# Kernel tuning notes

Measured on AMD Instinct MI355X. Metric: run time of the kernel, lower is better.

Reference implementation:

```python
import jax, jax.numpy as jnp
import numpy as np

B, L, E, H = 2, 2048, 1024, 16
HD = E // H  # 64
THETA = 10000.0


def setup_inputs() -> dict:
    key = jax.random.key(0)
    ks = jax.random.split(key, 9)
    s = 1.0 / np.sqrt(E)
    return {
        "x": jax.random.normal(ks[0], (B, L, E), jnp.float32),
        "Wq": jax.random.normal(ks[1], (E, E), jnp.float32) * s,
        "bq": jax.random.normal(ks[2], (E,), jnp.float32) * 0.01,
        "Wk": jax.random.normal(ks[3], (E, E), jnp.float32) * s,
        "bk": jax.random.normal(ks[4], (E,), jnp.float32) * 0.01,
        "Wv": jax.random.normal(ks[5], (E, E), jnp.float32) * s,
        "bv": jax.random.normal(ks[6], (E,), jnp.float32) * 0.01,
        "Wo": jax.random.normal(ks[7], (E, E), jnp.float32) * s,
        "bo": jax.random.normal(ks[8], (E,), jnp.float32) * 0.01,
    }


def _rope_tables(seq_len, dim, dtype):
    # lucidrains RotaryEmbedding: inv_freq over even indices, each freq repeated twice (interleaved)
    inv_freq = 1.0 / (THETA ** (jnp.arange(0, dim, 2, dtype=jnp.float32) / dim))
    freqs = jnp.arange(seq_len, dtype=jnp.float32)[:, None] * inv_freq[None, :]  # [L, dim/2]
    freqs = jnp.repeat(freqs, 2, axis=-1)  # [L, dim] -> f0,f0,f1,f1,...
    return jnp.cos(freqs).astype(dtype), jnp.sin(freqs).astype(dtype)


def _rotate_half(x):
    # interleaved pairs (x0, x1) -> (-x1, x0)
    x2 = x.reshape(*x.shape[:-1], -1, 2)
    x2 = jnp.stack([-x2[..., 1], x2[..., 0]], axis=-1)
    return x2.reshape(x.shape)


def _apply_rope(x, cos, sin):
    # x: [B, H, L, HD]; cos/sin: [L, HD]
    return x * cos[None, None] + _rotate_half(x) * sin[None, None]


def reference(x, Wq, bq, Wk, bk, Wv, bv, Wo, bo):
    b, l, e = x.shape
    q = (x @ Wq.T + bq).reshape(b, l, H, HD).transpose(0, 2, 1, 3)
    k = (x @ Wk.T + bk).reshape(b, l, H, HD).transpose(0, 2, 1, 3)
    v = (x @ Wv.T + bv).reshape(b, l, H, HD).transpose(0, 2, 1, 3)

    cos, sin = _rope_tables(l, HD, x.dtype)
    q = _apply_rope(q, cos, sin)
    k = _apply_rope(k, cos, sin)

    scale = 1.0 / np.sqrt(HD)
    scores = jnp.einsum("bhsd,bhed->bhse", q, k) * scale  # [B,H,L,L]
    attn = jax.nn.softmax(scores, axis=-1)
    out = jnp.einsum("bhse,bhed->bhsd", attn, v)  # [B,H,L,HD]
    out = out.transpose(0, 2, 1, 3).reshape(b, l, e)
    return out @ Wo.T + bo
```

## Files before the change

kernel.cpp:

```cpp
#include <hip/hip_runtime.h>

typedef unsigned short u16;
typedef __bf16 bf16x8 __attribute__((ext_vector_type(8)));
typedef float f32x4 __attribute__((ext_vector_type(4)));

#define LOG2E 1.4426950408889634f
#define EXP2(x) __builtin_amdgcn_exp2f(x)
#define NFM (-11.0f * LOG2E)

__device__ __forceinline__ u16 f2bf(float f) {
  unsigned int u = __float_as_uint(f);
  u += 0x7fffu + ((u >> 16) & 1u);
  return (u16)(u >> 16);
}

__device__ __forceinline__ void gld16(u16* lds, const u16* g) {
  __builtin_amdgcn_global_load_lds((const __attribute__((address_space(1))) unsigned int*)g,
                                   (__attribute__((address_space(3))) unsigned int*)lds,
                                   16, 0, 0);
}

__device__ __forceinline__ bf16x8 ldsv(const u16* p) {
  return *(const bf16x8*)p;
}

union U8 { uint4 u; bf16x8 v; };

__global__ __launch_bounds__(256) void k_prep(const float* __restrict__ x,
    const float* __restrict__ wq, const float* __restrict__ wk,
    const float* __restrict__ wv, const float* __restrict__ wo,
    u16* __restrict__ xb, u16* __restrict__ wqkvb, u16* __restrict__ wob,
    float* __restrict__ cosT, float* __restrict__ sinT) {
  unsigned gid = blockIdx.x * 256u + threadIdx.x;
  if (gid >= 2097152u) {
    unsigned t = gid - 2097152u;
    int l = t >> 5, i = t & 31;
    float inv = powf(10000.0f, -(float)i * (1.0f / 32.0f));
    float ang = (float)l * inv;
    float s, c;
    sincosf(ang, &s, &c);
    cosT[t] = c;
    sinT[t] = s;
    return;
  }
  const float4* src;
  u16* dst;
  unsigned off;
  if (gid < 1048576u)      { src = (const float4*)x;  dst = xb;              off = gid; }
  else if (gid < 1310720u) { src = (const float4*)wq; dst = wqkvb;           off = gid - 1048576u; }
  else if (gid < 1572864u) { src = (const float4*)wk; dst = wqkvb + 1048576; off = gid - 1310720u; }
  else if (gid < 1835008u) { src = (const float4*)wv; dst = wqkvb + 2097152; off = gid - 1572864u; }
  else                     { src = (const float4*)wo; dst = wob;             off = gid - 1835008u; }
  float4 f = src[off];
  ushort4 o;
  o.x = f2bf(f.x); o.y = f2bf(f.y); o.z = f2bf(f.z); o.w = f2bf(f.w);
  ((ushort4*)dst)[off] = o;
}

__device__ __forceinline__ void stage_tile(const u16* __restrict__ A, const u16* __restrict__ B,
                                           int m0, int n0, int kb, u16* dst) {
  const int tid = threadIdx.x;
#pragma unroll
  for (int it = 0; it < 4; ++it) {
    int idx = it * 256 + tid;
    int row = idx >> 3, c8 = idx & 7;
    int sc = c8 ^ (row & 7);
    gld16(dst + idx * 8,        A + (long)(m0 + row) * 1024 + kb + sc * 8);
    gld16(dst + 8192 + idx * 8, B + (long)(n0 + row) * 1024 + kb + sc * 8);
  }
}

__device__ __forceinline__ void gemm_loop(const u16* __restrict__ A, const u16* __restrict__ B,
                                          int m0, int n0, u16* S, f32x4 acc[4][4]) {
  const int tid = threadIdx.x;
  const int lane = tid & 63, wave = tid >> 6;
  const int quad = lane >> 4, l16 = lane & 15;
  const int wm = wave & 1, wn = wave >> 1;
  const int sw = l16 & 7;

#pragma unroll
  for (int i = 0; i < 4; ++i)
#pragma unroll
    for (int j = 0; j < 4; ++j)
      acc[i][j] = (f32x4){0.f, 0.f, 0.f, 0.f};

  stage_tile(A, B, m0, n0, 0, S);
  __syncthreads();

  for (int kt = 0; kt < 16; ++kt) {
    const int off = (kt & 1) << 14;
    const u16* As = S + off;
    const u16* Bs = S + off + 8192;
    if (kt < 15)
      stage_tile(A, B, m0, n0, (kt + 1) * 64, S + (off ^ 16384));
#pragma unroll
    for (int kk = 0; kk < 2; ++kk) {
      int ch = (kk * 4 + quad) ^ sw;
      bf16x8 a[4], b[4];
#pragma unroll
      for (int i = 0; i < 4; ++i)
        a[i] = ldsv(As + (wm * 64 + i * 16 + l16) * 64 + ch * 8);
#pragma unroll
      for (int j = 0; j < 4; ++j)
        b[j] = ldsv(Bs + (wn * 64 + j * 16 + l16) * 64 + ch * 8);
#pragma unroll
      for (int i = 0; i < 4; ++i)
#pragma unroll
        for (int j = 0; j < 4; ++j)
          acc[i][j] = __builtin_amdgcn_mfma_f32_16x16x32_bf16(a[i], b[j], acc[i][j], 0, 0, 0);
    }
    __syncthreads();
  }
}

__global__ __launch_bounds__(256) void k_qkv(const u16* __restrict__ xb, const u16* __restrict__ wqkvb,
    const float* __restrict__ bq, const float* __restrict__ bk, const float* __restrict__ bv,
    const float* __restrict__ cosT, const float* __restrict__ sinT,
    u16* __restrict__ Qg, u16* __restrict__ Kg, u16* __restrict__ VTg) {
  __shared__ __align__(16) u16 S[32768];
  f32x4 acc[4][4];
  int m0 = blockIdx.y * 128, n0 = blockIdx.x * 128;
  gemm_loop(xb, wqkvb, m0, n0, S, acc);

  const int tid = threadIdx.x, lane = tid & 63, wave = tid >> 6;
  const int quad = lane >> 4, l16 = lane & 15;
  const int wm = wave & 1, wn = wave >> 1;
  const int qsel = n0 >> 10;
  const int b = m0 >> 11;
  const int mb0 = m0 & 2047;

  if (qsel < 2) {
    const float* bp = qsel ? bk : bq;
#pragma unroll
    for (int j = 0; j < 4; ++j) {
      int nl = wn * 64 + j * 16 + l16;
      int n = n0 + nl;
      int fcol = n & 1023;
      int d = fcol & 63;
      int pi = d >> 1;
      float bias = bp[fcol];
      float sgn = (d & 1) ? 1.0f : -1.0f;
#pragma unroll
      for (int i = 0; i < 4; ++i) {
#pragma unroll
        for (int r = 0; r < 4; ++r) {
          int ml = wm * 64 + i * 16 + quad * 4 + r;
          int l = mb0 + ml;
          float v = acc[i][j][r] + bias;
          float partner = __shfl_xor(v, 1);
          float c = cosT[l * 32 + pi], s = sinT[l * 32 + pi];
          float o = fmaf(v, c, sgn * partner * s);
          if (qsel == 0) o *= 0.125f;
          S[ml * 132 + nl] = f2bf(o);
        }
      }
    }
    __syncthreads();
    u16* dstb = (qsel == 0) ? Qg : Kg;
#pragma unroll
    for (int t = 0; t < 16; ++t) {
      int idx = t * 256 + tid;
      int ml = idx >> 5, c4 = idx & 31;
      int n = n0 + c4 * 4;
      int h = (n & 1023) >> 6;
      int d = n & 63;
      *(uint2*)(dstb + (((long)b * 16 + h) * 2048 + mb0 + ml) * 64 + d) =
          *(const uint2*)(S + ml * 132 + c4 * 4);
    }
  } else {
#pragma unroll
    for (int j = 0; j < 4; ++j) {
      int nl = wn * 64 + j * 16 + l16;
      float bias = bv[(n0 + nl) & 1023];
#pragma unroll
      for (int i = 0; i < 4; ++i) {
        int mb = wm * 64 + i * 16 + quad * 4;
        unsigned u0 = (unsigned)f2bf(acc[i][j][0] + bias) | ((unsigned)f2bf(acc[i][j][1] + bias) << 16);
        unsigned u1 = (unsigned)f2bf(acc[i][j][2] + bias) | ((unsigned)f2bf(acc[i][j][3] + bias) << 16);
        *(uint2*)(S + nl * 132 + mb) = make_uint2(u0, u1);
      }
    }
    __syncthreads();
#pragma unroll
    for (int t = 0; t < 16; ++t) {
      int idx = t * 256 + tid;
      int nl = idx >> 5, c4 = idx & 31;
      int vcol = (n0 & 1023) + nl;
      int h = vcol >> 6, d = vcol & 63;
      *(uint2*)(VTg + (((long)b * 16 + h) * 64 + d) * 2048 + mb0 + c4 * 4) =
          *(const uint2*)(S + nl * 132 + c4 * 4);
    }
  }
}

__global__ __launch_bounds__(256, 2) void k_attn(const u16* __restrict__ Qg, const u16* __restrict__ Kg,
    const u16* __restrict__ VTg, u16* __restrict__ Ctx) {
  __shared__ __align__(16) char smem[65536];
  u16* Ks = (u16*)smem;
  u16* Vs0 = (u16*)(smem + 32768);
  const int tid = threadIdx.x, lane = tid & 63, wave = tid >> 6;
  const int quad = lane >> 4, l16 = lane & 15;
  const int wm = wave & 1, wsn = wave >> 1;
  const int sw = l16 & 7;
  const int bh = blockIdx.y;
  const int m0 = blockIdx.x * 128;
  const u16* Qb = Qg + (long)bh * 2048 * 64;
  const u16* Kb = Kg + (long)bh * 2048 * 64;
  const u16* Vb = VTg + (long)bh * 64 * 2048;

  bf16x8 qf[4][2];
#pragma unroll
  for (int mt = 0; mt < 4; ++mt)
#pragma unroll
    for (int kk = 0; kk < 2; ++kk)
      qf[mt][kk] = *(const bf16x8*)(Qb + (long)(m0 + wm * 64 + mt * 16 + l16) * 64 + kk * 32 + quad * 8);

  U8 ones;
  {
    unsigned w = (l16 == 0) ? 0x3F803F80u : 0u;
    ones.u = make_uint4(w, w, w, w);
  }
  const f32x4 zero4 = {0.f, 0.f, 0.f, 0.f};

  f32x4 oacc[4][4];
  f32x4 racc[4];
#pragma unroll
  for (int dt = 0; dt < 4; ++dt)
#pragma unroll
    for (int mt = 0; mt < 4; ++mt)
      oacc[dt][mt] = (f32x4){0.f, 0.f, 0.f, 0.f};
#pragma unroll
  for (int mt = 0; mt < 4; ++mt) racc[mt] = (f32x4){0.f, 0.f, 0.f, 0.f};

  const int r7 = l16 & 7;
  const int qh = quad >> 1;
  const int qo = (quad & 1) * 4;

#pragma unroll
  for (int it = 0; it < 4; ++it) {
    int idx = it * 256 + tid;
    int row = idx >> 4, c16 = idx & 15;
    int sc = (c16 & 8) | ((c16 & 7) ^ (row & 7));
    gld16(Vs0 + idx * 8, Vb + (long)row * 2048 + sc * 8);
  }
#pragma unroll
  for (int it = 0; it < 4; ++it) {
    int idx = it * 256 + tid;
    int row = idx >> 3, c8 = idx & 7;
    int sc = c8 ^ (row & 7);
    gld16(Ks + idx * 8, Kb + (long)row * 64 + sc * 8);
  }
  __syncthreads();

  for (int st = 0; st < 16; ++st) {
    const int cur = st & 1;
    const u16* Ksc = Ks + cur * 8192;
    u16* Ksa = Ks + (cur ^ 1) * 8192;
    const u16* Vsc = Vs0 + cur * 8192;
    u16* Vsa = Vs0 + (cur ^ 1) * 8192;

    if (st < 15) {
      int s0n = (st + 1) * 128;
#pragma unroll
      for (int it = 0; it < 4; ++it) {
        int idx = it * 256 + tid;
        int row = idx >> 4, c16 = idx & 15;
        int sc = (c16 & 8) | ((c16 & 7) ^ (row & 7));
        gld16(Vsa + idx * 8, Vb + (long)row * 2048 + s0n + sc * 8);
      }
#pragma unroll
      for (int it = 0; it < 4; ++it) {
        int idx = it * 256 + tid;
        int row = idx >> 3, c8 = idx & 7;
        int sc = c8 ^ (row & 7);
        gld16(Ksa + idx * 8, Kb + (long)(s0n + row) * 64 + sc * 8);
      }
    }

    f32x4 sacc[4][4];
    {
      int ch = quad ^ sw;
      bf16x8 kf[4];
#pragma unroll
      for (int ct = 0; ct < 4; ++ct)
        kf[ct] = ldsv(Ksc + (wsn * 64 + ct * 16 + l16) * 64 + ch * 8);
#pragma unroll
      for (int ct = 0; ct < 4; ++ct)
#pragma unroll
        for (int mt = 0; mt < 4; ++mt)
          sacc[ct][mt] = __builtin_amdgcn_mfma_f32_16x16x32_bf16(kf[ct], qf[mt][0], zero4, 0, 0, 0);
    }
    {
      int ch = (4 + quad) ^ sw;
      bf16x8 kf[4];
#pragma unroll
      for (int ct = 0; ct < 4; ++ct)
        kf[ct] = ldsv(Ksc + (wsn * 64 + ct * 16 + l16) * 64 + ch * 8);
#pragma unroll
      for (int ct = 0; ct < 4; ++ct)
#pragma unroll
        for (int mt = 0; mt < 4; ++mt)
          sacc[ct][mt] = __builtin_amdgcn_mfma_f32_16x16x32_bf16(kf[ct], qf[mt][1], sacc[ct][mt], 0, 0, 0);
    }

#pragma unroll
    for (int c = 0; c < 2; ++c) {
      unsigned pk[2][4][2];
#pragma unroll
      for (int t = 0; t < 2; ++t) {
        int ct = c * 2 + t;
#pragma unroll
        for (int mt = 0; mt < 4; ++mt) {
          unsigned b[4];
#pragma unroll
          for (int r = 0; r < 4; ++r) {
            float e = EXP2(fmaf(sacc[ct][mt][r], LOG2E, NFM));
            b[r] = __float_as_uint(e);
          }
          pk[t][mt][0] = __builtin_amdgcn_perm(b[1], b[0], 0x07060302u);
          pk[t][mt][1] = __builtin_amdgcn_perm(b[3], b[2], 0x07060302u);
        }
      }
      const int slo = (4 * c + qh) ^ r7;
      const int shi = (4 * c + qh + 2) ^ r7;
#pragma unroll
      for (int dt = 0; dt < 4; ++dt) {
        const u16* vrow = Vsc + (dt * 16 + l16) * 128 + wsn * 64;
        uint2 lo = *(const uint2*)(vrow + slo * 8 + qo);
        uint2 hi = *(const uint2*)(vrow + shi * 8 + qo);
        U8 vfu; vfu.u = make_uint4(lo.x, lo.y, hi.x, hi.y);
#pragma unroll
        for (int mt = 0; mt < 4; ++mt) {
          U8 pfu; pfu.u = make_uint4(pk[0][mt][0], pk[0][mt][1], pk[1][mt][0], pk[1][mt][1]);
          oacc[dt][mt] = __builtin_amdgcn_mfma_f32_16x16x32_bf16(vfu.v, pfu.v, oacc[dt][mt], 0, 0, 0);
        }
      }
#pragma unroll
      for (int mt = 0; mt < 4; ++mt) {
        U8 pfu; pfu.u = make_uint4(pk[0][mt][0], pk[0][mt][1], pk[1][mt][0], pk[1][mt][1]);
        racc[mt] = __builtin_amdgcn_mfma_f32_16x16x32_bf16(ones.v, pfu.v, racc[mt], 0, 0, 0);
      }
    }

    __syncthreads();
  }

  float rs[4];
#pragma unroll
  for (int mt = 0; mt < 4; ++mt) rs[mt] = racc[mt][0];

  float* mbuf = (float*)smem;
  if (wsn == 1) {
#pragma unroll
    for (int dt = 0; dt < 4; ++dt)
#pragma unroll
      for (int mt = 0; mt < 4; ++mt)
#pragma unroll
        for (int r = 0; r < 4; ++r)
          mbuf[(wm * 68 + dt * 16 + mt * 4 + r) * 64 + lane] = oacc[dt][mt][r];
#pragma unroll
    for (int mt = 0; mt < 4; ++mt)
      mbuf[(wm * 68 + 64 + mt) * 64 + lane] = rs[mt];
  }
  __syncthreads();
  if (wsn == 0) {
#pragma unroll
    for (int dt = 0; dt < 4; ++dt)
#pragma unroll
      for (int mt = 0; mt < 4; ++mt)
#pragma unroll
        for (int r = 0; r < 4; ++r)
          oacc[dt][mt][r] += mbuf[(wm * 68 + dt * 16 + mt * 4 + r) * 64 + lane];
#pragma unroll
    for (int mt = 0; mt < 4; ++mt) {
      rs[mt] += mbuf[(wm * 68 + 64 + mt) * 64 + lane];
      rs[mt] += __shfl_xor(rs[mt], 16);
      rs[mt] += __shfl_xor(rs[mt], 32);
    }
    const int b = bh >> 4, h = bh & 15;
#pragma unroll
    for (int mt = 0; mt < 4; ++mt) {
      float inv = 1.0f / rs[mt];
      int tok = m0 + wm * 64 + mt * 16 + l16;
      u16* cp = Ctx + ((long)(b * 2048 + tok)) * 1024 + h * 64 + quad * 4;
#pragma unroll
      for (int dt = 0; dt < 4; ++dt) {
        float o0 = oacc[dt][mt][0] * inv, o1 = oacc[dt][mt][1] * inv;
        float o2 = oacc[dt][mt][2] * inv, o3 = oacc[dt][mt][3] * inv;
        unsigned u0 = (unsigned)f2bf(o0) | ((unsigned)f2bf(o1) << 16);
        unsigned u1 = (unsigned)f2bf(o2) | ((unsigned)f2bf(o3) << 16);
        *(uint2*)(cp + dt * 16) = make_uint2(u0, u1);
      }
    }
  }
}

__device__ __forceinline__ void stage_tile64(const u16* __restrict__ A, const u16* __restrict__ B,
                                             int m0, int n0, int kb, u16* dst) {
  const int tid = threadIdx.x;
#pragma unroll
  for (int it = 0; it < 2; ++it) {
    int idx = it * 256 + tid;
    int row = idx >> 3, c8 = idx & 7;
    int sc = c8 ^ (row & 7);
    gld16(dst + idx * 8, A + (long)(m0 + row) * 1024 + kb + sc * 8);
  }
#pragma unroll
  for (int it = 0; it < 4; ++it) {
    int idx = it * 256 + tid;
    int row = idx >> 3, c8 = idx & 7;
    int sc = c8 ^ (row & 7);
    gld16(dst + 4096 + idx * 8, B + (long)(n0 + row) * 1024 + kb + sc * 8);
  }
}

__global__ __launch_bounds__(256) void k_out(const u16* __restrict__ Ctx, const u16* __restrict__ wob,
    const float* __restrict__ bo, float* __restrict__ out) {
  __shared__ __align__(16) u16 S[24576];
  const int tid = threadIdx.x, lane = tid & 63, wave = tid >> 6;
  const int quad = lane >> 4, l16 = lane & 15;
  const int wm = wave & 1, wn = wave >> 1;
  const int sw = l16 & 7;
  int m0 = blockIdx.y * 64, n0 = blockIdx.x * 128;

  f32x4 acc[2][4];
#pragma unroll
  for (int i = 0; i < 2; ++i)
#pragma unroll
    for (int j = 0; j < 4; ++j)
      acc[i][j] = (f32x4){0.f, 0.f, 0.f, 0.f};

  stage_tile64(Ctx, wob, m0, n0, 0, S);
  __syncthreads();

  for (int kt = 0; kt < 16; ++kt) {
    const int off = (kt & 1) * 12288;
    const u16* As = S + off;
    const u16* Bs = S + off + 4096;
    if (kt < 15)
      stage_tile64(Ctx, wob, m0, n0, (kt + 1) * 64, S + (off ^ 12288));
#pragma unroll
    for (int kk = 0; kk < 2; ++kk) {
      int ch = (kk * 4 + quad) ^ sw;
      bf16x8 a[2], b[4];
#pragma unroll
      for (int i = 0; i < 2; ++i)
        a[i] = ldsv(As + (wm * 32 + i * 16 + l16) * 64 + ch * 8);
#pragma unroll
      for (int j = 0; j < 4; ++j)
        b[j] = ldsv(Bs + (wn * 64 + j * 16 + l16) * 64 + ch * 8);
#pragma unroll
      for (int i = 0; i < 2; ++i)
#pragma unroll
        for (int j = 0; j < 4; ++j)
          acc[i][j] = __builtin_amdgcn_mfma_f32_16x16x32_bf16(a[i], b[j], acc[i][j], 0, 0, 0);
    }
    __syncthreads();
  }

#pragma unroll
  for (int i = 0; i < 2; ++i)
#pragma unroll
    for (int j = 0; j < 4; ++j) {
      int n = n0 + wn * 64 + j * 16 + l16;
      float b_ = bo[n];
#pragma unroll
      for (int r = 0; r < 4; ++r) {
        int m = m0 + wm * 32 + i * 16 + quad * 4 + r;
        out[(long)m * 1024 + n] = acc[i][j][r] + b_;
      }
    }
}

extern "C" void kernel_launch(void* const* d_in, const int* in_sizes, int n_in,
                              void* d_out, int out_size, void* d_ws, size_t ws_size,
                              hipStream_t stream) {
  const float* x  = (const float*)d_in[0];
  const float* Wq = (const float*)d_in[1];
  const float* bq = (const float*)d_in[2];
  const float* Wk = (const float*)d_in[3];
  const float* bk = (const float*)d_in[4];
  const float* Wv = (const float*)d_in[5];
  const float* bv = (const float*)d_in[6];
  const float* Wo = (const float*)d_in[7];
  const float* bo = (const float*)d_in[8];
  float* out = (float*)d_out;

  char* ws = (char*)d_ws;
  u16* xb    = (u16*)(ws);
  u16* wqkvb = (u16*)(ws + (8ul << 20));
  u16* wob   = (u16*)(ws + (14ul << 20));
  u16* Qg    = (u16*)(ws + (16ul << 20));
  u16* Kg    = (u16*)(ws + (24ul << 20));
  u16* VTg   = (u16*)(ws + (32ul << 20));
  u16* Ctx   = (u16*)(ws + (40ul << 20));
  float* cosT = (float*)(ws + (48ul << 20));
  float* sinT = (float*)(ws + (48ul << 20) + (256ul << 10));

  k_prep<<<dim3(8448), dim3(256), 0, stream>>>(x, Wq, Wk, Wv, Wo, xb, wqkvb, wob, cosT, sinT);
  k_qkv<<<dim3(24, 32), dim3(256), 0, stream>>>(xb, wqkvb, bq, bk, bv, cosT, sinT, Qg, Kg, VTg);
  k_attn<<<dim3(16, 32), dim3(256), 0, stream>>>(Qg, Kg, VTg, Ctx);
  k_out<<<dim3(8, 64), dim3(256), 0, stream>>>(Ctx, wob, bo, out);
}
```

Before: 186.7 us.

## Use triple-buffered BK=32 pipeline with vmcnt waits in QKV GEMM

```diff
diff --git a/kernel.cpp b/kernel.cpp
--- a/kernel.cpp
+++ b/kernel.cpp
@@ -57,26 +57,33 @@
   ((ushort4*)dst)[off] = o;
 }
 
-__device__ __forceinline__ void stage_tile(const u16* __restrict__ A, const u16* __restrict__ B,
-                                           int m0, int n0, int kb, u16* dst) {
+__device__ __forceinline__ void stage32(const u16* __restrict__ A, const u16* __restrict__ B,
+                                        int m0, int n0, int kb, u16* dst) {
   const int tid = threadIdx.x;
 #pragma unroll
-  for (int it = 0; it < 4; ++it) {
+  for (int it = 0; it < 2; ++it) {
     int idx = it * 256 + tid;
-    int row = idx >> 3, c8 = idx & 7;
-    int sc = c8 ^ (row & 7);
-    gld16(dst + idx * 8,        A + (long)(m0 + row) * 1024 + kb + sc * 8);
-    gld16(dst + 8192 + idx * 8, B + (long)(n0 + row) * 1024 + kb + sc * 8);
-  }
-}
-
-__device__ __forceinline__ void gemm_loop(const u16* __restrict__ A, const u16* __restrict__ B,
-                                          int m0, int n0, u16* S, f32x4 acc[4][4]) {
+    int row = idx >> 2, c4 = idx & 3;
+    int sc = c4 ^ ((row >> 1) & 3);
+    gld16(dst + idx * 8, A + (long)(m0 + row) * 1024 + kb + sc * 8);
+  }
+#pragma unroll
+  for (int it = 0; it < 2; ++it) {
+    int idx = it * 256 + tid;
+    int row = idx >> 2, c4 = idx & 3;
+    int sc = c4 ^ ((row >> 1) & 3);
+    gld16(dst + 4096 + idx * 8, B + (long)(n0 + row) * 1024 + kb + sc * 8);
+  }
+}
+
+__device__ __forceinline__ void gemm_loop32(const u16* __restrict__ A, const u16* __restrict__ B,
+                                            int m0, int n0, u16* S, f32x4 acc[4][4]) {
   const int tid = threadIdx.x;
   const int lane = tid & 63, wave = tid >> 6;
   const int quad = lane >> 4, l16 = lane & 15;
   const int wm = wave & 1, wn = wave >> 1;
-  const int sw = l16 & 7;
+  const int sw2 = (l16 >> 1) & 3;
+  const int ch = quad ^ sw2;
 
 #pragma unroll
   for (int i = 0; i < 4; ++i)
@@ -84,32 +91,34 @@
     for (int j = 0; j < 4; ++j)
       acc[i][j] = (f32x4){0.f, 0.f, 0.f, 0.f};
 
-  stage_tile(A, B, m0, n0, 0, S);
-  __syncthreads();
-
-  for (int kt = 0; kt < 16; ++kt) {
-    const int off = (kt & 1) << 14;
-    const u16* As = S + off;
-    const u16* Bs = S + off + 8192;
-    if (kt < 15)
-      stage_tile(A, B, m0, n0, (kt + 1) * 64, S + (off ^ 16384));
-#pragma unroll
-    for (int kk = 0; kk < 2; ++kk) {
-      int ch = (kk * 4 + quad) ^ sw;
-      bf16x8 a[4], b[4];
-#pragma unroll
-      for (int i = 0; i < 4; ++i)
-        a[i] = ldsv(As + (wm * 64 + i * 16 + l16) * 64 + ch * 8);
+  stage32(A, B, m0, n0, 0, S);
+  stage32(A, B, m0, n0, 32, S + 8192);
+
+  int bc = 0;
+  for (int kt = 0; kt < 32; ++kt) {
+    if (kt < 31) { asm volatile("s_waitcnt vmcnt(4)" ::: "memory"); }
+    else         { asm volatile("s_waitcnt vmcnt(0)" ::: "memory"); }
+    __builtin_amdgcn_sched_barrier(0);
+    __builtin_amdgcn_s_barrier();
+    if (kt < 30) {
+      int bs = (bc == 0) ? 2 : bc - 1;
+      stage32(A, B, m0, n0, (kt + 2) * 32, S + bs * 8192);
+    }
+    const u16* As = S + bc * 8192;
+    const u16* Bs = As + 4096;
+    bf16x8 a[4], b[4];
+#pragma unroll
+    for (int i = 0; i < 4; ++i)
+      a[i] = ldsv(As + (wm * 64 + i * 16 + l16) * 32 + ch * 8);
+#pragma unroll
+    for (int j = 0; j < 4; ++j)
+      b[j] = ldsv(Bs + (wn * 64 + j * 16 + l16) * 32 + ch * 8);
+#pragma unroll
+    for (int i = 0; i < 4; ++i)
 #pragma unroll
       for (int j = 0; j < 4; ++j)
-        b[j] = ldsv(Bs + (wn * 64 + j * 16 + l16) * 64 + ch * 8);
-#pragma unroll
-      for (int i = 0; i < 4; ++i)
-#pragma unroll
-        for (int j = 0; j < 4; ++j)
-          acc[i][j] = __builtin_amdgcn_mfma_f32_16x16x32_bf16(a[i], b[j], acc[i][j], 0, 0, 0);
-    }
-    __syncthreads();
+        acc[i][j] = __builtin_amdgcn_mfma_f32_16x16x32_bf16(a[i], b[j], acc[i][j], 0, 0, 0);
+    bc = (bc == 2) ? 0 : bc + 1;
   }
 }
 
@@ -117,10 +126,11 @@
     const float* __restrict__ bq, const float* __restrict__ bk, const float* __restrict__ bv,
     const float* __restrict__ cosT, const float* __restrict__ sinT,
     u16* __restrict__ Qg, u16* __restrict__ Kg, u16* __restrict__ VTg) {
-  __shared__ __align__(16) u16 S[32768];
+  __shared__ __align__(16) u16 S[24576];
   f32x4 acc[4][4];
   int m0 = blockIdx.y * 128, n0 = blockIdx.x * 128;
-  gemm_loop(xb, wqkvb, m0, n0, S, acc);
+  gemm_loop32(xb, wqkvb, m0, n0, S, acc);
+  __syncthreads();
 
   const int tid = threadIdx.x, lane = tid & 63, wave = tid >> 6;
   const int quad = lane >> 4, l16 = lane & 15;
```

After: 184.5 us. No clear change (-1.2%).
